# Optimization experiments

Hardware: AMD Instinct MI355X
Metric: run time of the kernel (lower is better)

Reference implementation:

```python
import jax, jax.numpy as jnp
import numpy as np

D_MODEL = 256
N_LAYERS = 2
EXPAND = 2
D_INNER = EXPAND * D_MODEL  # 512
D_STATE = 16
D_CONV = 4
DT_RANK = max(1, D_MODEL // 16)  # 16


def _selective_scan(x, dt, B, C, A, D):
    # x, dt: [b, l, d]   B, C: [b, l, n]   A: [d, n]   D: [d]
    dA = jnp.exp(jnp.einsum('bld,dn->bldn', dt, A))          # discretized state matrix
    dBx = jnp.einsum('bld,bln,bld->bldn', dt, B, x)           # dt * B * u

    def step(h, inp):
        dA_t, dBx_t, C_t = inp                                 # [b,d,n],[b,d,n],[b,n]
        h = dA_t * h + dBx_t
        y = jnp.einsum('bdn,bn->bd', h, C_t)
        return h, y

    h0 = jnp.zeros((x.shape[0], A.shape[0], A.shape[1]), x.dtype)
    _, ys = jax.lax.scan(step, h0, (jnp.moveaxis(dA, 1, 0),
                                    jnp.moveaxis(dBx, 1, 0),
                                    jnp.moveaxis(C, 1, 0)))
    return jnp.moveaxis(ys, 0, 1) + x * D                      # [b, l, d]


def _mamba_block(z, in_w, conv_w, conv_b, xp_w, dt_w, dt_b, A_log, Dp, out_w):
    b, l, _ = z.shape
    xz = z @ in_w.T                                            # [b, l, 2*d_inner]
    x, gate = jnp.split(xz, 2, axis=-1)
    # causal depthwise conv1d over time
    xt = jnp.transpose(x, (0, 2, 1))                            # [b, d_inner, l]
    xt = jax.lax.conv_general_dilated(
        xt, conv_w[:, None, :], window_strides=(1,),
        padding=[(D_CONV - 1, 0)], feature_group_count=D_INNER)
    x = jax.nn.silu(jnp.transpose(xt, (0, 2, 1)) + conv_b)      # [b, l, d_inner]
    x_dbl = x @ xp_w.T                                          # [b, l, dt_rank + 2*d_state]
    dt, Bm, Cm = jnp.split(x_dbl, [DT_RANK, DT_RANK + D_STATE], axis=-1)
    dt = jax.nn.softplus(dt @ dt_w.T + dt_b)                    # [b, l, d_inner]
    A = -jnp.exp(A_log)                                         # [d_inner, d_state]
    y = _selective_scan(x, dt, Bm, Cm, A, Dp)
    y = y * jax.nn.silu(gate)
    return y @ out_w.T                                          # [b, l, d_model]


def setup_inputs() -> dict:
    key = jax.random.key(0)
    ks = jax.random.split(key, 9)
    B, L = 2, 4096
    z = jax.random.normal(ks[0], (B, L, D_MODEL), jnp.float32)
    s = 0.02
    in_proj_w = jax.random.normal(ks[1], (N_LAYERS, 2 * D_INNER, D_MODEL), jnp.float32) * s
    conv_w = jax.random.normal(ks[2], (N_LAYERS, D_INNER, D_CONV), jnp.float32) * 0.2
    conv_b = jnp.zeros((N_LAYERS, D_INNER), jnp.float32)
    x_proj_w = jax.random.normal(ks[3], (N_LAYERS, DT_RANK + 2 * D_STATE, D_INNER), jnp.float32) * s
    dt_proj_w = jax.random.normal(ks[4], (N_LAYERS, D_INNER, DT_RANK), jnp.float32) * 0.1
    dt_proj_b = jax.random.uniform(ks[5], (N_LAYERS, D_INNER), jnp.float32, -4.0, -2.0)
    A_log = jnp.log(jnp.broadcast_to(jnp.arange(1, D_STATE + 1, dtype=jnp.float32),
                                     (N_LAYERS, D_INNER, D_STATE)))
    D_param = jnp.ones((N_LAYERS, D_INNER), jnp.float32)
    out_proj_w = jax.random.normal(ks[6], (N_LAYERS, D_MODEL, D_INNER), jnp.float32) * s
    return {"z": z, "in_proj_w": in_proj_w, "conv_w": conv_w, "conv_b": conv_b,
            "x_proj_w": x_proj_w, "dt_proj_w": dt_proj_w, "dt_proj_b": dt_proj_b,
            "A_log": A_log, "D_param": D_param, "out_proj_w": out_proj_w}


def reference(z, in_proj_w, conv_w, conv_b, x_proj_w, dt_proj_w, dt_proj_b,
              A_log, D_param, out_proj_w):
    for i in range(N_LAYERS):
        z = _mamba_block(z, in_proj_w[i], conv_w[i], conv_b[i], x_proj_w[i],
                         dt_proj_w[i], dt_proj_b[i], A_log[i], D_param[i], out_proj_w[i])
    return z
```

## Files before the change

### kernel.cpp

```cpp
#include <hip/hip_runtime.h>
#include <hip/hip_bf16.h>
#include <cstdint>
#include <cstddef>

#define DM   256
#define DI   512
#define DS   16
#define LSEQ 4096
#define BATCH 2
#define BLROWS (BATCH * LSEQ)
#define NCH  256
#define CLEN 16
#define NSC  16
#define XCP  520
#define ASP  264

typedef __bf16 bf16x8 __attribute__((ext_vector_type(8)));
typedef float  f32x4  __attribute__((ext_vector_type(4)));
typedef unsigned short u16;
typedef u16 u16x8 __attribute__((ext_vector_type(8)));

__device__ __forceinline__ u16 f2bfu(float f) {
    union { float f; unsigned u; } c; c.f = f;
    unsigned u = c.u;
    return (u16)((u + 0x7fffu + ((u >> 16) & 1u)) >> 16);
}
__device__ __forceinline__ float bfu2f(u16 u) {
    union { unsigned u; float f; } c; c.u = ((unsigned)u) << 16; return c.f;
}
__device__ __forceinline__ float siluf(float v) {
    return v * (1.0f / (1.0f + __expf(-v)));
}

#define N_INW  (2*1024*256)
#define N_OUTW (2*256*512)
#define N_XPW  (2*64*512)
#define N_Z    (BLROWS*DM)
__global__ __launch_bounds__(256) void cast_all_k(
    const float* __restrict__ in_w, const float* __restrict__ out_w,
    const float* __restrict__ xp_w, const float* __restrict__ z,
    u16* __restrict__ inw_bf, u16* __restrict__ outw_bf,
    u16* __restrict__ xpw_bf, u16* __restrict__ z_bf) {
    int i = blockIdx.x * 256 + threadIdx.x;
    if (i < N_INW) {
        inw_bf[i] = f2bfu(in_w[i]);
    } else if (i < N_INW + N_OUTW) {
        int j = i - N_INW;
        outw_bf[j] = f2bfu(out_w[j]);
    } else if (i < N_INW + N_OUTW + N_XPW) {
        int j = i - (N_INW + N_OUTW);
        int k = j & 511, o = (j >> 9) & 63, l = j >> 15;
        xpw_bf[j] = f2bfu((o < 48) ? xp_w[(l * 48 + o) * 512 + k] : 0.0f);
    } else {
        int j = i - (N_INW + N_OUTW + N_XPW);
        z_bf[j] = f2bfu(z[j]);
    }
}

__global__ __launch_bounds__(256, 2) void gemm_in_k(
    const __bf16* __restrict__ A, const __bf16* __restrict__ B,
    u16* __restrict__ Cb) {
    __shared__ u16 As[64 * ASP];
    int tid = threadIdx.x, wave = tid >> 6, lane = tid & 63;
    int bm = blockIdx.x * 64, bn = blockIdx.y * 256 + wave * 64;
    int row = lane & 15, q = lane >> 4;

    {
        int col = (tid & 31) * 8;
        #pragma unroll
        for (int i = 0; i < 8; ++i) {
            int r = i * 8 + (tid >> 5);
            u16x8 v = *(const u16x8*)((const u16*)A + (size_t)(bm + r) * 256 + col);
            *(u16x8*)&As[r * ASP + col] = v;
        }
    }
    __syncthreads();

    f32x4 acc[4][4] = {};
    for (int k = 0; k < 8; ++k) {
        bf16x8 af[4], bfr[4];
        #pragma unroll
        for (int mi = 0; mi < 4; ++mi)
            af[mi] = *(const bf16x8*)&As[(mi*16 + row) * ASP + k*32 + q*8];
        #pragma unroll
        for (int ni = 0; ni < 4; ++ni)
            bfr[ni] = *(const bf16x8*)(B + (size_t)(bn + ni*16 + row) * 256 + k*32 + q*8);
        #pragma unroll
        for (int mi = 0; mi < 4; ++mi)
            #pragma unroll
            for (int ni = 0; ni < 4; ++ni)
                acc[mi][ni] = __builtin_amdgcn_mfma_f32_16x16x32_bf16(
                    af[mi], bfr[ni], acc[mi][ni], 0, 0, 0);
    }
    #pragma unroll
    for (int mi = 0; mi < 4; ++mi)
        #pragma unroll
        for (int r = 0; r < 4; ++r) {
            size_t gr = (size_t)(bm + mi*16 + q*4 + r) * 1024;
            #pragma unroll
            for (int ni = 0; ni < 4; ++ni)
                Cb[gr + bn + ni*16 + row] = f2bfu(acc[mi][ni][r]);
        }
}

__global__ __launch_bounds__(512, 4) void fused_a_k(
    const u16* __restrict__ xz, const float* __restrict__ cw,
    const float* __restrict__ cb, const __bf16* __restrict__ xpw,
    const float* __restrict__ dtw, const float* __restrict__ dtb,
    const float* __restrict__ Alog,
    u16* __restrict__ xcb, u16* __restrict__ dtob,
    float* __restrict__ BCg, u16* __restrict__ Pb, u16* __restrict__ Sb) {
    __shared__ u16 xc_s[CLEN * XCP];
    __shared__ float xd_h[2][CLEN * 68];
    int tid = threadIdx.x;
    int c = blockIdx.x, b = blockIdx.y;
    int flat = b * NCH + c;
    int bl0 = b * LSEQ + c * CLEN;
    int d = tid;

    {
        float w0 = cw[d*4], w1 = cw[d*4+1], w2 = cw[d*4+2], w3 = cw[d*4+3];
        float bias = cb[d];
        float xm3 = 0.f, xm2 = 0.f, xm1 = 0.f;
        int l0 = c * CLEN;
        if (l0 - 3 >= 0) xm3 = bfu2f(xz[(size_t)(bl0 - 3) * 1024 + d]);
        if (l0 - 2 >= 0) xm2 = bfu2f(xz[(size_t)(bl0 - 2) * 1024 + d]);
        if (l0 - 1 >= 0) xm1 = bfu2f(xz[(size_t)(bl0 - 1) * 1024 + d]);
        #pragma unroll 4
        for (int t = 0; t < CLEN; ++t) {
            float xcur = bfu2f(xz[(size_t)(bl0 + t) * 1024 + d]);
            float acc = fmaf(w0, xm3, fmaf(w1, xm2, fmaf(w2, xm1, fmaf(w3, xcur, bias))));
            float v = siluf(acc);
            u16 vb = f2bfu(v);
            xc_s[t * XCP + d] = vb;
            xcb[(size_t)(bl0 + t) * DI + d] = vb;
            xm3 = xm2; xm2 = xm1; xm1 = xcur;
        }
    }
    __syncthreads();

    {
        int wave = tid >> 6, lane = tid & 63;
        int row = lane & 15, q = lane >> 4;
        int nt = wave & 3, kh = wave >> 2;
        f32x4 acc = {0.f, 0.f, 0.f, 0.f};
        #pragma unroll
        for (int kb = 0; kb < 8; ++kb) {
            int kk = (kh*8 + kb) * 32;
            bf16x8 a = *(const bf16x8*)&xc_s[row * XCP + kk + q*8];
            bf16x8 bb = *(const bf16x8*)(xpw + (size_t)(nt*16 + row) * 512 + kk + q*8);
            acc = __builtin_amdgcn_mfma_f32_16x16x32_bf16(a, bb, acc, 0, 0, 0);
        }
        #pragma unroll
        for (int r = 0; r < 4; ++r)
            xd_h[kh][(q*4 + r) * 68 + nt*16 + row] = acc[r];
    }
    __syncthreads();
    for (int j = tid; j < CLEN * 68; j += 512) xd_h[0][j] += xd_h[1][j];
    __syncthreads();

    {
        int t = tid >> 5, cc = tid & 31;
        BCg[(size_t)flat * (CLEN*32) + tid] = xd_h[0][t*68 + 16 + cc];
    }

    {
        float dtwr[16];
        const f32x4* w4 = (const f32x4*)(dtw + (size_t)d * 16);
        #pragma unroll
        for (int g = 0; g < 4; ++g) { f32x4 v = w4[g];
            dtwr[g*4] = v[0]; dtwr[g*4+1] = v[1]; dtwr[g*4+2] = v[2]; dtwr[g*4+3] = v[3]; }
        float dtbv = dtb[d];
        float Ac[16];
        const f32x4* a4 = (const f32x4*)(Alog + (size_t)d * 16);
        #pragma unroll
        for (int g = 0; g < 4; ++g) { f32x4 v = a4[g];
            #pragma unroll
            for (int j = 0; j < 4; ++j) Ac[g*4+j] = -__expf(v[j]); }
        bool fastp = true;
        #pragma unroll
        for (int n = 1; n < 16; ++n)
            fastp = fastp && (fabsf(Ac[n] - (float)(n+1) * Ac[0])
                              <= 1e-4f * fabsf(Ac[n]));
        float p[16], s[16];
        #pragma unroll
        for (int n = 0; n < 16; ++n) { p[n] = 1.0f; s[n] = 0.0f; }
        for (int t = 0; t < CLEN; ++t) {
            float acc = dtbv;
            #pragma unroll
            for (int r = 0; r < 16; ++r) acc = fmaf(xd_h[0][t*68 + r], dtwr[r], acc);
            float dtraw = (acc > 20.0f) ? acc : logf(1.0f + __expf(acc));
            float dtv = bfu2f(f2bfu(dtraw));
            dtob[(size_t)(bl0 + t) * DI + d] = f2bfu(dtraw);
            float xv = bfu2f(xc_s[t * XCP + d]);
            float dx = dtv * xv;
            float an[16];
            if (fastp) {
                float a0 = __expf(dtv * Ac[0]);
                an[0] = a0;
                #pragma unroll
                for (int n = 1; n < 16; ++n) an[n] = an[n-1] * a0;
            } else {
                #pragma unroll
                for (int n = 0; n < 16; ++n) an[n] = __expf(dtv * Ac[n]);
            }
            #pragma unroll
            for (int n = 0; n < 16; ++n) {
                s[n] = fmaf(an[n], s[n], xd_h[0][t*68 + 16 + n] * dx);
                p[n] *= an[n];
            }
        }
        size_t base = ((size_t)flat * DI + d) * 16;
        u16x8 pv0, pv1, sv0, sv1;
        #pragma unroll
        for (int n = 0; n < 8; ++n) {
            pv0[n] = f2bfu(p[n]);   pv1[n] = f2bfu(p[8+n]);
            sv0[n] = f2bfu(s[n]);   sv1[n] = f2bfu(s[8+n]);
        }
        *(u16x8*)(Pb + base)     = pv0;  *(u16x8*)(Pb + base + 8) = pv1;
        *(u16x8*)(Sb + base)     = sv0;  *(u16x8*)(Sb + base + 8) = sv1;
    }
}

__global__ __launch_bounds__(256) void scan1_k(
    const u16* __restrict__ Pb, const u16* __restrict__ Sb,
    float* __restrict__ Pagg, float* __restrict__ Sagg) {
    int gid = blockIdx.x * 256 + threadIdx.x;
    int scg = gid >> 13, elow = gid & 8191;
    int b = scg >> 4, sc = scg & 15;
    int cbase = b * NCH + sc * 16;
    float h = 0.f, p = 1.f;
    #pragma unroll
    for (int k = 0; k < 16; ++k) {
        size_t a = (size_t)(cbase + k) * 8192 + elow;
        float Pv = bfu2f(Pb[a]), Sv = bfu2f(Sb[a]);
        h = fmaf(Pv, h, Sv);
        p *= Pv;
    }
    Pagg[(size_t)scg * 8192 + elow] = p;
    Sagg[(size_t)scg * 8192 + elow] = h;
}

__global__ __launch_bounds__(256) void scan2_k(
    const u16* __restrict__ Pb, const u16* __restrict__ Sb,
    const float* __restrict__ Pagg, const float* __restrict__ Sagg,
    u16* __restrict__ Hg) {
    int gid = blockIdx.x * 256 + threadIdx.x;
    int scg = gid >> 13, elow = gid & 8191;
    int b = scg >> 4, sc = scg & 15;
    int cbase = b * NCH + sc * 16;
    float h = 0.f;
    for (int s2 = 0; s2 < sc; ++s2) {
        size_t ai = (size_t)(b*16 + s2) * 8192 + elow;
        h = fmaf(Pagg[ai], h, Sagg[ai]);
    }
    #pragma unroll
    for (int k = 0; k < 16; ++k) {
        size_t a = (size_t)(cbase + k) * 8192 + elow;
        Hg[a] = f2bfu(h);
        h = fmaf(bfu2f(Pb[a]), h, bfu2f(Sb[a]));
    }
}

__global__ __launch_bounds__(512, 4) void fused_c_k(
    const u16* __restrict__ xcb, const u16* __restrict__ dtob,
    const float* __restrict__ BCg, const u16* __restrict__ Hg,
    const float* __restrict__ Alog, const float* __restrict__ Dp,
    const u16* __restrict__ xz, const __bf16* __restrict__ outw,
    u16* __restrict__ Ob, float* __restrict__ Of) {
    __shared__ u16 y_s[CLEN * XCP];
    __shared__ float BCs[CLEN * 32];
    int tid = threadIdx.x;
    int c = blockIdx.x, b = blockIdx.y;
    int flat = b * NCH + c;
    int bl0 = b * LSEQ + c * CLEN;
    int d = tid;

    BCs[tid] = BCg[(size_t)flat * (CLEN*32) + tid];

    float Ac[16], h[16];
    {
        const f32x4* a4 = (const f32x4*)(Alog + (size_t)d * 16);
        const u16* h8 = Hg + ((size_t)flat * DI + d) * 16;
        u16x8 hv0 = *(const u16x8*)h8;
        u16x8 hv1 = *(const u16x8*)(h8 + 8);
        #pragma unroll
        for (int g = 0; g < 4; ++g) {
            f32x4 av = a4[g];
            #pragma unroll
            for (int j = 0; j < 4; ++j) Ac[g*4+j] = -__expf(av[j]);
        }
        #pragma unroll
        for (int n = 0; n < 8; ++n) { h[n] = bfu2f(hv0[n]); h[8+n] = bfu2f(hv1[n]); }
    }
    bool fastp = true;
    #pragma unroll
    for (int n = 1; n < 16; ++n)
        fastp = fastp && (fabsf(Ac[n] - (float)(n+1) * Ac[0]) <= 1e-4f * fabsf(Ac[n]));
    float Dv = Dp[d];
    __syncthreads();

    #pragma unroll 4
    for (int t = 0; t < CLEN; ++t) {
        float dtv = bfu2f(dtob[(size_t)(bl0 + t) * DI + d]);
        float xv  = bfu2f(xcb[(size_t)(bl0 + t) * DI + d]);
        float gv  = bfu2f(xz[(size_t)(bl0 + t) * 1024 + DI + d]);
        float dx = dtv * xv;
        float an[16];
        if (fastp) {
            float a0 = __expf(dtv * Ac[0]);
            an[0] = a0;
            #pragma unroll
            for (int n = 1; n < 16; ++n) an[n] = an[n-1] * a0;
        } else {
            #pragma unroll
            for (int n = 0; n < 16; ++n) an[n] = __expf(dtv * Ac[n]);
        }
        float y = 0.f;
        #pragma unroll
        for (int n = 0; n < 16; ++n) {
            h[n] = fmaf(an[n], h[n], BCs[t*32 + n] * dx);
            y = fmaf(h[n], BCs[t*32 + 16 + n], y);
        }
        float yv = fmaf(xv, Dv, y) * siluf(gv);
        y_s[t * XCP + d] = f2bfu(yv);
    }
    __syncthreads();

    {
        int wave = tid >> 6, lane = tid & 63;
        int row = lane & 15, q = lane >> 4;
        f32x4 acc[2] = {};
        #pragma unroll
        for (int kb = 0; kb < 16; ++kb) {
            bf16x8 a = *(const bf16x8*)&y_s[row * XCP + kb*32 + q*8];
            #pragma unroll
            for (int ni = 0; ni < 2; ++ni) {
                bf16x8 bb = *(const bf16x8*)(outw +
                    (size_t)(wave*32 + ni*16 + row) * 512 + kb*32 + q*8);
                acc[ni] = __builtin_amdgcn_mfma_f32_16x16x32_bf16(a, bb, acc[ni], 0, 0, 0);
            }
        }
        #pragma unroll
        for (int r = 0; r < 4; ++r) {
            size_t gr = (size_t)(bl0 + q*4 + r) * DM;
            #pragma unroll
            for (int ni = 0; ni < 2; ++ni) {
                int gc = wave*32 + ni*16 + row;
                if (Ob) Ob[gr + gc] = f2bfu(acc[ni][r]);
                else    Of[gr + gc] = acc[ni][r];
            }
        }
    }
}

extern "C" void kernel_launch(void* const* d_in, const int* in_sizes, int n_in,
                              void* d_out, int out_size, void* d_ws, size_t ws_size,
                              hipStream_t stream) {
    (void)in_sizes; (void)n_in; (void)out_size; (void)ws_size;
    const float* z_in   = (const float*)d_in[0];
    const float* in_w   = (const float*)d_in[1];
    const float* conv_w = (const float*)d_in[2];
    const float* conv_b = (const float*)d_in[3];
    const float* xp_w   = (const float*)d_in[4];
    const float* dt_w   = (const float*)d_in[5];
    const float* dt_b   = (const float*)d_in[6];
    const float* A_log  = (const float*)d_in[7];
    const float* D_par  = (const float*)d_in[8];
    const float* out_w  = (const float*)d_in[9];
    float* outp = (float*)d_out;

    char* p = (char*)d_ws;
    auto alloc = [&](size_t bytes) { char* r = p; p += (bytes + 255) & ~(size_t)255; return r; };
    u16* z_bf    = (u16*)alloc((size_t)BLROWS*DM*2);
    u16* z2_bf   = (u16*)alloc((size_t)BLROWS*DM*2);
    u16* xz_bf   = (u16*)alloc((size_t)BLROWS*1024*2);
    u16* xc_bf   = (u16*)alloc((size_t)BLROWS*DI*2);
    u16* dt_bf   = (u16*)alloc((size_t)BLROWS*DI*2);
    u16* inw_bf  = (u16*)alloc((size_t)2*1024*256*2);
    u16* outw_bf = (u16*)alloc((size_t)2*256*512*2);
    u16* xpw_bf  = (u16*)alloc((size_t)2*64*512*2);
    float* BCg   = (float*)alloc((size_t)BATCH*NCH*CLEN*32*4);
    u16* Pbuf    = (u16*)alloc((size_t)BATCH*NCH*DI*DS*2);
    u16* Sbuf    = (u16*)alloc((size_t)BATCH*NCH*DI*DS*2);
    u16* Hbuf    = (u16*)alloc((size_t)BATCH*NCH*DI*DS*2);
    float* PaggG = (float*)alloc((size_t)BATCH*NSC*8192*4);
    float* SaggG = (float*)alloc((size_t)BATCH*NSC*8192*4);

    cast_all_k<<<(N_INW + N_OUTW + N_XPW + N_Z)/256, 256, 0, stream>>>(
        in_w, out_w, xp_w, z_in, inw_bf, outw_bf, xpw_bf, z_bf);

    const u16* zcur = z_bf;
    for (int l = 0; l < 2; ++l) {
        gemm_in_k<<<dim3(BLROWS/64, 1024/256), 256, 0, stream>>>(
            (const __bf16*)zcur, (const __bf16*)(inw_bf + (size_t)l*1024*256),
            xz_bf);
        fused_a_k<<<dim3(NCH, BATCH), 512, 0, stream>>>(
            xz_bf, conv_w + (size_t)l*DI*4, conv_b + (size_t)l*DI,
            (const __bf16*)(xpw_bf + (size_t)l*64*512),
            dt_w + (size_t)l*DI*16, dt_b + (size_t)l*DI,
            A_log + (size_t)l*DI*DS,
            xc_bf, dt_bf, BCg, Pbuf, Sbuf);
        scan1_k<<<BATCH*NSC*8192/256, 256, 0, stream>>>(Pbuf, Sbuf, PaggG, SaggG);
        scan2_k<<<BATCH*NSC*8192/256, 256, 0, stream>>>(Pbuf, Sbuf, PaggG, SaggG, Hbuf);
        fused_c_k<<<dim3(NCH, BATCH), 512, 0, stream>>>(
            xc_bf, dt_bf, BCg, Hbuf,
            A_log + (size_t)l*DI*DS, D_par + (size_t)l*DI,
            xz_bf, (const __bf16*)(outw_bf + (size_t)l*256*512),
            (l == 0) ? z2_bf : nullptr, (l == 1) ? outp : nullptr);
        zcur = z2_bf;
    }
}
```

Before: 234.5 us.

## Split fused scan kernels into separate conv, GEMM, dt, scan stages

Breaks the two large fused per-chunk kernels into separate conv, x-projection GEMM, dt, chunk-scan and output-GEMM kernels. It also halves the chunk length and doubles the chunk count, splits channels across two blocks per chunk, and computes the chunk decay product in closed form from the summed dt with a power tree. The aim is more parallel blocks, lower register pressure and shorter serial dependency chains. In exchange it adds extra launches and global round-trips for xd and the y intermediate, and doubles the chunk-state buffers that scan1/scan2 must process.

```diff
diff --git a/kernel.cpp b/kernel.cpp
--- a/kernel.cpp
+++ b/kernel.cpp
@@ -9,10 +9,9 @@
 #define LSEQ 4096
 #define BATCH 2
 #define BLROWS (BATCH * LSEQ)
-#define NCH  256
-#define CLEN 16
-#define NSC  16
-#define XCP  520
+#define NCH  512
+#define CLEN 8
+#define NSC  32
 #define ASP  264
 
 typedef __bf16 bf16x8 __attribute__((ext_vector_type(8)));
@@ -31,6 +30,13 @@
 __device__ __forceinline__ float siluf(float v) {
     return v * (1.0f / (1.0f + __expf(-v)));
 }
+
+#define POW_TREE(an, e1)                                                     \
+    {   float e2 = (e1)*(e1), e4 = e2*e2, e8 = e4*e4;                        \
+        an[0]=(e1); an[1]=e2; an[2]=e2*(e1); an[3]=e4; an[4]=e4*(e1);        \
+        an[5]=e4*e2; an[6]=e4*an[2]; an[7]=e8; an[8]=e8*(e1); an[9]=e8*e2;   \
+        an[10]=e8*an[2]; an[11]=e8*e4; an[12]=e8*an[4]; an[13]=e8*an[5];     \
+        an[14]=e8*an[6]; an[15]=e8*e8; }
 
 #define N_INW  (2*1024*256)
 #define N_OUTW (2*256*512)
@@ -64,7 +70,6 @@
     int tid = threadIdx.x, wave = tid >> 6, lane = tid & 63;
     int bm = blockIdx.x * 64, bn = blockIdx.y * 256 + wave * 64;
     int row = lane & 15, q = lane >> 4;
-
     {
         int col = (tid & 31) * 8;
         #pragma unroll
@@ -75,7 +80,6 @@
         }
     }
     __syncthreads();
-
     f32x4 acc[4][4] = {};
     for (int k = 0; k < 8; ++k) {
         bf16x8 af[4], bfr[4];
@@ -103,123 +107,137 @@
         }
 }
 
-__global__ __launch_bounds__(512, 4) void fused_a_k(
+__global__ __launch_bounds__(256) void conv_k(
     const u16* __restrict__ xz, const float* __restrict__ cw,
-    const float* __restrict__ cb, const __bf16* __restrict__ xpw,
-    const float* __restrict__ dtw, const float* __restrict__ dtb,
-    const float* __restrict__ Alog,
-    u16* __restrict__ xcb, u16* __restrict__ dtob,
-    float* __restrict__ BCg, u16* __restrict__ Pb, u16* __restrict__ Sb) {
-    __shared__ u16 xc_s[CLEN * XCP];
-    __shared__ float xd_h[2][CLEN * 68];
+    const float* __restrict__ cb, u16* __restrict__ xc) {
+    int gid = blockIdx.x * 256 + threadIdx.x;
+    int d = gid & 511;
+    int row0 = (gid >> 9) * 8;
+    int l0 = row0 & 4095;
+    float w0 = cw[d*4], w1 = cw[d*4+1], w2 = cw[d*4+2], w3 = cw[d*4+3];
+    float bias = cb[d];
+    float xm3 = (l0 >= 3) ? bfu2f(xz[(size_t)(row0-3)*1024 + d]) : 0.f;
+    float xm2 = (l0 >= 2) ? bfu2f(xz[(size_t)(row0-2)*1024 + d]) : 0.f;
+    float xm1 = (l0 >= 1) ? bfu2f(xz[(size_t)(row0-1)*1024 + d]) : 0.f;
+    #pragma unroll
+    for (int t = 0; t < 8; ++t) {
+        float xcur = bfu2f(xz[(size_t)(row0+t)*1024 + d]);
+        float a = fmaf(w0, xm3, fmaf(w1, xm2, fmaf(w2, xm1, fmaf(w3, xcur, bias))));
+        xc[(size_t)(row0+t)*512 + d] = f2bfu(siluf(a));
+        xm3 = xm2; xm2 = xm1; xm1 = xcur;
+    }
+}
+
+__global__ __launch_bounds__(256) void gemm_xd_k(
+    const __bf16* __restrict__ xc, const __bf16* __restrict__ xpw,
+    float* __restrict__ xd) {
+    int tid = threadIdx.x, wave = tid >> 6, lane = tid & 63;
+    int bm = blockIdx.x * 16;
+    int row = lane & 15, q = lane >> 4;
+    f32x4 acc = {};
+    #pragma unroll
+    for (int k = 0; k < 16; ++k) {
+        bf16x8 a = *(const bf16x8*)(xc + (size_t)(bm + row)*512 + k*32 + q*8);
+        bf16x8 b = *(const bf16x8*)(xpw + (size_t)(wave*16 + row)*512 + k*32 + q*8);
+        acc = __builtin_amdgcn_mfma_f32_16x16x32_bf16(a, b, acc, 0, 0, 0);
+    }
+    #pragma unroll
+    for (int r = 0; r < 4; ++r)
+        xd[(size_t)(bm + q*4 + r)*64 + wave*16 + row] = acc[r];
+}
+
+__global__ __launch_bounds__(256) void dt_k(
+    const float* __restrict__ xd, const float* __restrict__ dtw,
+    const float* __restrict__ dtb, u16* __restrict__ dt) {
+    int gid = blockIdx.x * 256 + threadIdx.x;
+    int d = gid & 511, t = gid >> 9;
+    const f32x4* w4 = (const f32x4*)(dtw + (size_t)d*16);
+    const f32x4* x4 = (const f32x4*)(xd + (size_t)t*64);
+    float acc = dtb[d];
+    #pragma unroll
+    for (int g = 0; g < 4; ++g) {
+        f32x4 wv = w4[g], xv = x4[g];
+        #pragma unroll
+        for (int j = 0; j < 4; ++j) acc = fmaf(xv[j], wv[j], acc);
+    }
+    float dtraw = (acc > 20.0f) ? acc : __logf(1.0f + __expf(acc));
+    dt[gid] = f2bfu(dtraw);
+}
+
+__global__ __launch_bounds__(256, 6) void scan_ps_k(
+    const u16* __restrict__ xc, const u16* __restrict__ dt,
+    const float* __restrict__ xd, const float* __restrict__ Alog,
+    u16* __restrict__ Pb, u16* __restrict__ Sb) {
+    __shared__ float BCs[CLEN * 32];
     int tid = threadIdx.x;
-    int c = blockIdx.x, b = blockIdx.y;
+    int c = blockIdx.x, bh = blockIdx.y;
+    int b = bh >> 1, dch = (bh & 1) * 256 + tid;
     int flat = b * NCH + c;
     int bl0 = b * LSEQ + c * CLEN;
-    int d = tid;
-
+    BCs[tid] = xd[(size_t)(bl0 + (tid >> 5)) * 64 + 16 + (tid & 31)];
+    float Ac0; bool fastp = true;
     {
-        float w0 = cw[d*4], w1 = cw[d*4+1], w2 = cw[d*4+2], w3 = cw[d*4+3];
-        float bias = cb[d];
-        float xm3 = 0.f, xm2 = 0.f, xm1 = 0.f;
-        int l0 = c * CLEN;
-        if (l0 - 3 >= 0) xm3 = bfu2f(xz[(size_t)(bl0 - 3) * 1024 + d]);
-        if (l0 - 2 >= 0) xm2 = bfu2f(xz[(size_t)(bl0 - 2) * 1024 + d]);
-        if (l0 - 1 >= 0) xm1 = bfu2f(xz[(size_t)(bl0 - 1) * 1024 + d]);
-        #pragma unroll 4
+        const f32x4* a4 = (const f32x4*)(Alog + (size_t)dch * 16);
+        f32x4 v0 = a4[0];
+        Ac0 = -__expf(v0[0]);
+        #pragma unroll
+        for (int g = 0; g < 4; ++g) { f32x4 v = a4[g];
+            #pragma unroll
+            for (int j = 0; j < 4; ++j) { int n = g*4 + j; if (n) {
+                float acn = -__expf(v[j]);
+                fastp = fastp && (fabsf(acn - (float)(n+1)*Ac0) <= 1e-4f*fabsf(acn));
+            } } }
+    }
+    __syncthreads();
+    float s[16];
+    #pragma unroll
+    for (int n = 0; n < 16; ++n) s[n] = 0.f;
+    float Sdt = 0.f;
+    if (fastp) {
+        #pragma unroll
         for (int t = 0; t < CLEN; ++t) {
-            float xcur = bfu2f(xz[(size_t)(bl0 + t) * 1024 + d]);
-            float acc = fmaf(w0, xm3, fmaf(w1, xm2, fmaf(w2, xm1, fmaf(w3, xcur, bias))));
-            float v = siluf(acc);
-            u16 vb = f2bfu(v);
-            xc_s[t * XCP + d] = vb;
-            xcb[(size_t)(bl0 + t) * DI + d] = vb;
-            xm3 = xm2; xm2 = xm1; xm1 = xcur;
-        }
-    }
-    __syncthreads();
-
-    {
-        int wave = tid >> 6, lane = tid & 63;
-        int row = lane & 15, q = lane >> 4;
-        int nt = wave & 3, kh = wave >> 2;
-        f32x4 acc = {0.f, 0.f, 0.f, 0.f};
-        #pragma unroll
-        for (int kb = 0; kb < 8; ++kb) {
-            int kk = (kh*8 + kb) * 32;
-            bf16x8 a = *(const bf16x8*)&xc_s[row * XCP + kk + q*8];
-            bf16x8 bb = *(const bf16x8*)(xpw + (size_t)(nt*16 + row) * 512 + kk + q*8);
-            acc = __builtin_amdgcn_mfma_f32_16x16x32_bf16(a, bb, acc, 0, 0, 0);
-        }
-        #pragma unroll
-        for (int r = 0; r < 4; ++r)
-            xd_h[kh][(q*4 + r) * 68 + nt*16 + row] = acc[r];
-    }
-    __syncthreads();
-    for (int j = tid; j < CLEN * 68; j += 512) xd_h[0][j] += xd_h[1][j];
-    __syncthreads();
-
-    {
-        int t = tid >> 5, cc = tid & 31;
-        BCg[(size_t)flat * (CLEN*32) + tid] = xd_h[0][t*68 + 16 + cc];
-    }
-
-    {
-        float dtwr[16];
-        const f32x4* w4 = (const f32x4*)(dtw + (size_t)d * 16);
-        #pragma unroll
-        for (int g = 0; g < 4; ++g) { f32x4 v = w4[g];
-            dtwr[g*4] = v[0]; dtwr[g*4+1] = v[1]; dtwr[g*4+2] = v[2]; dtwr[g*4+3] = v[3]; }
-        float dtbv = dtb[d];
-        float Ac[16];
-        const f32x4* a4 = (const f32x4*)(Alog + (size_t)d * 16);
-        #pragma unroll
-        for (int g = 0; g < 4; ++g) { f32x4 v = a4[g];
-            #pragma unroll
-            for (int j = 0; j < 4; ++j) Ac[g*4+j] = -__expf(v[j]); }
-        bool fastp = true;
-        #pragma unroll
-        for (int n = 1; n < 16; ++n)
-            fastp = fastp && (fabsf(Ac[n] - (float)(n+1) * Ac[0])
-                              <= 1e-4f * fabsf(Ac[n]));
-        float p[16], s[16];
-        #pragma unroll
-        for (int n = 0; n < 16; ++n) { p[n] = 1.0f; s[n] = 0.0f; }
+            float dtv = bfu2f(dt[(size_t)(bl0+t)*512 + dch]);
+            float xv  = bfu2f(xc[(size_t)(bl0+t)*512 + dch]);
+            float dx = dtv * xv;
+            Sdt += dtv;
+            float e1 = __expf(dtv * Ac0);
+            float an[16];
+            POW_TREE(an, e1)
+            #pragma unroll
+            for (int n = 0; n < 16; ++n)
+                s[n] = fmaf(an[n], s[n], BCs[t*32 + n] * dx);
+        }
+    } else {
         for (int t = 0; t < CLEN; ++t) {
-            float acc = dtbv;
-            #pragma unroll
-            for (int r = 0; r < 16; ++r) acc = fmaf(xd_h[0][t*68 + r], dtwr[r], acc);
-            float dtraw = (acc > 20.0f) ? acc : logf(1.0f + __expf(acc));
-            float dtv = bfu2f(f2bfu(dtraw));
-            dtob[(size_t)(bl0 + t) * DI + d] = f2bfu(dtraw);
-            float xv = bfu2f(xc_s[t * XCP + d]);
+            float dtv = bfu2f(dt[(size_t)(bl0+t)*512 + dch]);
+            float xv  = bfu2f(xc[(size_t)(bl0+t)*512 + dch]);
             float dx = dtv * xv;
-            float an[16];
-            if (fastp) {
-                float a0 = __expf(dtv * Ac[0]);
-                an[0] = a0;
-                #pragma unroll
-                for (int n = 1; n < 16; ++n) an[n] = an[n-1] * a0;
-            } else {
-                #pragma unroll
-                for (int n = 0; n < 16; ++n) an[n] = __expf(dtv * Ac[n]);
+            Sdt += dtv;
+            #pragma unroll
+            for (int n = 0; n < 16; ++n) {
+                float an = __expf(dtv * -__expf(Alog[(size_t)dch*16 + n]));
+                s[n] = fmaf(an, s[n], BCs[t*32 + n] * dx);
             }
-            #pragma unroll
-            for (int n = 0; n < 16; ++n) {
-                s[n] = fmaf(an[n], s[n], xd_h[0][t*68 + 16 + n] * dx);
-                p[n] *= an[n];
-            }
-        }
-        size_t base = ((size_t)flat * DI + d) * 16;
-        u16x8 pv0, pv1, sv0, sv1;
-        #pragma unroll
-        for (int n = 0; n < 8; ++n) {
-            pv0[n] = f2bfu(p[n]);   pv1[n] = f2bfu(p[8+n]);
-            sv0[n] = f2bfu(s[n]);   sv1[n] = f2bfu(s[8+n]);
-        }
-        *(u16x8*)(Pb + base)     = pv0;  *(u16x8*)(Pb + base + 8) = pv1;
-        *(u16x8*)(Sb + base)     = sv0;  *(u16x8*)(Sb + base + 8) = sv1;
-    }
+        }
+    }
+    float pw[16];
+    if (fastp) {
+        float E1 = __expf(Ac0 * Sdt);
+        POW_TREE(pw, E1)
+    } else {
+        #pragma unroll
+        for (int n = 0; n < 16; ++n)
+            pw[n] = __expf(-__expf(Alog[(size_t)dch*16 + n]) * Sdt);
+    }
+    size_t base = ((size_t)flat * DI + dch) * 16;
+    u16x8 pv0, pv1, sv0, sv1;
+    #pragma unroll
+    for (int n = 0; n < 8; ++n) {
+        pv0[n] = f2bfu(pw[n]);  pv1[n] = f2bfu(pw[8+n]);
+        sv0[n] = f2bfu(s[n]);   sv1[n] = f2bfu(s[8+n]);
+    }
+    *(u16x8*)(Pb + base)     = pv0;  *(u16x8*)(Pb + base + 8) = pv1;
+    *(u16x8*)(Sb + base)     = sv0;  *(u16x8*)(Sb + base + 8) = sv1;
 }
 
 __global__ __launch_bounds__(256) void scan1_k(
@@ -227,7 +245,7 @@
     float* __restrict__ Pagg, float* __restrict__ Sagg) {
     int gid = blockIdx.x * 256 + threadIdx.x;
     int scg = gid >> 13, elow = gid & 8191;
-    int b = scg >> 4, sc = scg & 15;
+    int b = scg >> 5, sc = scg & 31;
     int cbase = b * NCH + sc * 16;
     float h = 0.f, p = 1.f;
     #pragma unroll
@@ -247,11 +265,11 @@
     u16* __restrict__ Hg) {
     int gid = blockIdx.x * 256 + threadIdx.x;
     int scg = gid >> 13, elow = gid & 8191;
-    int b = scg >> 4, sc = scg & 15;
+    int b = scg >> 5, sc = scg & 31;
     int cbase = b * NCH + sc * 16;
     float h = 0.f;
     for (int s2 = 0; s2 < sc; ++s2) {
-        size_t ai = (size_t)(b*16 + s2) * 8192 + elow;
+        size_t ai = (size_t)(b*32 + s2) * 8192 + elow;
         h = fmaf(Pagg[ai], h, Sagg[ai]);
     }
     #pragma unroll
@@ -262,94 +280,110 @@
     }
 }
 
-__global__ __launch_bounds__(512, 4) void fused_c_k(
-    const u16* __restrict__ xcb, const u16* __restrict__ dtob,
-    const float* __restrict__ BCg, const u16* __restrict__ Hg,
+__global__ __launch_bounds__(256, 6) void scan_y_k(
+    const u16* __restrict__ xc, const u16* __restrict__ dt,
+    const float* __restrict__ xd, const u16* __restrict__ Hg,
     const float* __restrict__ Alog, const float* __restrict__ Dp,
-    const u16* __restrict__ xz, const __bf16* __restrict__ outw,
-    u16* __restrict__ Ob, float* __restrict__ Of) {
-    __shared__ u16 y_s[CLEN * XCP];
+    const u16* __restrict__ xz, u16* __restrict__ yg) {
     __shared__ float BCs[CLEN * 32];
     int tid = threadIdx.x;
-    int c = blockIdx.x, b = blockIdx.y;
+    int c = blockIdx.x, bh = blockIdx.y;
+    int b = bh >> 1, dch = (bh & 1) * 256 + tid;
     int flat = b * NCH + c;
     int bl0 = b * LSEQ + c * CLEN;
-    int d = tid;
-
-    BCs[tid] = BCg[(size_t)flat * (CLEN*32) + tid];
-
-    float Ac[16], h[16];
+    BCs[tid] = xd[(size_t)(bl0 + (tid >> 5)) * 64 + 16 + (tid & 31)];
+    float Ac0; bool fastp = true;
     {
-        const f32x4* a4 = (const f32x4*)(Alog + (size_t)d * 16);
-        const u16* h8 = Hg + ((size_t)flat * DI + d) * 16;
+        const f32x4* a4 = (const f32x4*)(Alog + (size_t)dch * 16);
+        f32x4 v0 = a4[0];
+        Ac0 = -__expf(v0[0]);
+        #pragma unroll
+        for (int g = 0; g < 4; ++g) { f32x4 v = a4[g];
+            #pragma unroll
+            for (int j = 0; j < 4; ++j) { int n = g*4 + j; if (n) {
+                float acn = -__expf(v[j]);
+                fastp = fastp && (fabsf(acn - (float)(n+1)*Ac0) <= 1e-4f*fabsf(acn));
+            } } }
+    }
+    float h[16];
+    {
+        const u16* h8 = Hg + ((size_t)flat * DI + dch) * 16;
         u16x8 hv0 = *(const u16x8*)h8;
         u16x8 hv1 = *(const u16x8*)(h8 + 8);
         #pragma unroll
-        for (int g = 0; g < 4; ++g) {
-            f32x4 av = a4[g];
-            #pragma unroll
-            for (int j = 0; j < 4; ++j) Ac[g*4+j] = -__expf(av[j]);
-        }
-        #pragma unroll
         for (int n = 0; n < 8; ++n) { h[n] = bfu2f(hv0[n]); h[8+n] = bfu2f(hv1[n]); }
     }
-    bool fastp = true;
-    #pragma unroll
-    for (int n = 1; n < 16; ++n)
-        fastp = fastp && (fabsf(Ac[n] - (float)(n+1) * Ac[0]) <= 1e-4f * fabsf(Ac[n]));
-    float Dv = Dp[d];
+    float Dv = Dp[dch];
     __syncthreads();
-
-    #pragma unroll 4
-    for (int t = 0; t < CLEN; ++t) {
-        float dtv = bfu2f(dtob[(size_t)(bl0 + t) * DI + d]);
-        float xv  = bfu2f(xcb[(size_t)(bl0 + t) * DI + d]);
-        float gv  = bfu2f(xz[(size_t)(bl0 + t) * 1024 + DI + d]);
-        float dx = dtv * xv;
-        float an[16];
-        if (fastp) {
-            float a0 = __expf(dtv * Ac[0]);
-            an[0] = a0;
-            #pragma unroll
-            for (int n = 1; n < 16; ++n) an[n] = an[n-1] * a0;
-        } else {
-            #pragma unroll
-            for (int n = 0; n < 16; ++n) an[n] = __expf(dtv * Ac[n]);
-        }
-        float y = 0.f;
-        #pragma unroll
-        for (int n = 0; n < 16; ++n) {
-            h[n] = fmaf(an[n], h[n], BCs[t*32 + n] * dx);
-            y = fmaf(h[n], BCs[t*32 + 16 + n], y);
-        }
-        float yv = fmaf(xv, Dv, y) * siluf(gv);
-        y_s[t * XCP + d] = f2bfu(yv);
-    }
-    __syncthreads();
-
-    {
-        int wave = tid >> 6, lane = tid & 63;
-        int row = lane & 15, q = lane >> 4;
-        f32x4 acc[2] = {};
-        #pragma unroll
-        for (int kb = 0; kb < 16; ++kb) {
-            bf16x8 a = *(const bf16x8*)&y_s[row * XCP + kb*32 + q*8];
-            #pragma unroll
-            for (int ni = 0; ni < 2; ++ni) {
-                bf16x8 bb = *(const bf16x8*)(outw +
-                    (size_t)(wave*32 + ni*16 + row) * 512 + kb*32 + q*8);
-                acc[ni] = __builtin_amdgcn_mfma_f32_16x16x32_bf16(a, bb, acc[ni], 0, 0, 0);
+    if (fastp) {
+        #pragma unroll
+        for (int t = 0; t < CLEN; ++t) {
+            float dtv = bfu2f(dt[(size_t)(bl0+t)*512 + dch]);
+            float xv  = bfu2f(xc[(size_t)(bl0+t)*512 + dch]);
+            float gv  = bfu2f(xz[(size_t)(bl0+t)*1024 + DI + dch]);
+            float dx = dtv * xv;
+            float e1 = __expf(dtv * Ac0);
+            float an[16];
+            POW_TREE(an, e1)
+            float y0 = 0.f, y1 = 0.f, y2 = 0.f, y3 = 0.f;
+            #pragma unroll
+            for (int n = 0; n < 4; ++n) {
+                h[n]    = fmaf(an[n],    h[n],    BCs[t*32 + n]    * dx);
+                h[4+n]  = fmaf(an[4+n],  h[4+n],  BCs[t*32 + 4+n]  * dx);
+                h[8+n]  = fmaf(an[8+n],  h[8+n],  BCs[t*32 + 8+n]  * dx);
+                h[12+n] = fmaf(an[12+n], h[12+n], BCs[t*32 + 12+n] * dx);
+                y0 = fmaf(h[n],    BCs[t*32 + 16 + n],    y0);
+                y1 = fmaf(h[4+n],  BCs[t*32 + 16 + 4+n],  y1);
+                y2 = fmaf(h[8+n],  BCs[t*32 + 16 + 8+n],  y2);
+                y3 = fmaf(h[12+n], BCs[t*32 + 16 + 12+n], y3);
             }
-        }
-        #pragma unroll
-        for (int r = 0; r < 4; ++r) {
-            size_t gr = (size_t)(bl0 + q*4 + r) * DM;
-            #pragma unroll
-            for (int ni = 0; ni < 2; ++ni) {
-                int gc = wave*32 + ni*16 + row;
-                if (Ob) Ob[gr + gc] = f2bfu(acc[ni][r]);
-                else    Of[gr + gc] = acc[ni][r];
+            float y = (y0 + y1) + (y2 + y3);
+            float yv = fmaf(xv, Dv, y) * siluf(gv);
+            yg[(size_t)(bl0+t)*512 + dch] = f2bfu(yv);
+        }
+    } else {
+        for (int t = 0; t < CLEN; ++t) {
+            float dtv = bfu2f(dt[(size_t)(bl0+t)*512 + dch]);
+            float xv  = bfu2f(xc[(size_t)(bl0+t)*512 + dch]);
+            float gv  = bfu2f(xz[(size_t)(bl0+t)*1024 + DI + dch]);
+            float dx = dtv * xv;
+            float y = 0.f;
+            #pragma unroll
+            for (int n = 0; n < 16; ++n) {
+                float an = __expf(dtv * -__expf(Alog[(size_t)dch*16 + n]));
+                h[n] = fmaf(an, h[n], BCs[t*32 + n] * dx);
+                y = fmaf(h[n], BCs[t*32 + 16 + n], y);
             }
+            float yv = fmaf(xv, Dv, y) * siluf(gv);
+            yg[(size_t)(bl0+t)*512 + dch] = f2bfu(yv);
+        }
+    }
+}
+
+__global__ __launch_bounds__(256) void gemm_out_k(
+    const __bf16* __restrict__ yg, const __bf16* __restrict__ outw,
+    u16* __restrict__ Ob, float* __restrict__ Of) {
+    int tid = threadIdx.x, wave = tid >> 6, lane = tid & 63;
+    int bm = blockIdx.x * 16;
+    int row = lane & 15, q = lane >> 4;
+    f32x4 acc[4] = {};
+    #pragma unroll
+    for (int k = 0; k < 16; ++k) {
+        bf16x8 a = *(const bf16x8*)(yg + (size_t)(bm + row)*512 + k*32 + q*8);
+        #pragma unroll
+        for (int ni = 0; ni < 4; ++ni) {
+            bf16x8 b = *(const bf16x8*)(outw + (size_t)(wave*64 + ni*16 + row)*512 + k*32 + q*8);
+            acc[ni] = __builtin_amdgcn_mfma_f32_16x16x32_bf16(a, b, acc[ni], 0, 0, 0);
+        }
+    }
+    #pragma unroll
+    for (int r = 0; r < 4; ++r) {
+        size_t gr = (size_t)(bm + q*4 + r) * DM;
+        #pragma unroll
+        for (int ni = 0; ni < 4; ++ni) {
+            int gc = wave*64 + ni*16 + row;
+            if (Ob) Ob[gr + gc] = f2bfu(acc[ni][r]);
+            else    Of[gr + gc] = acc[ni][r];
         }
     }
 }
@@ -377,10 +411,11 @@
     u16* xz_bf   = (u16*)alloc((size_t)BLROWS*1024*2);
     u16* xc_bf   = (u16*)alloc((size_t)BLROWS*DI*2);
     u16* dt_bf   = (u16*)alloc((size_t)BLROWS*DI*2);
+    u16* yg_bf   = (u16*)alloc((size_t)BLROWS*DI*2);
+    float* xdG   = (float*)alloc((size_t)BLROWS*64*4);
     u16* inw_bf  = (u16*)alloc((size_t)2*1024*256*2);
     u16* outw_bf = (u16*)alloc((size_t)2*256*512*2);
     u16* xpw_bf  = (u16*)alloc((size_t)2*64*512*2);
-    float* BCg   = (float*)alloc((size_t)BATCH*NCH*CLEN*32*4);
     u16* Pbuf    = (u16*)alloc((size_t)BATCH*NCH*DI*DS*2);
     u16* Sbuf    = (u16*)alloc((size_t)BATCH*NCH*DI*DS*2);
     u16* Hbuf    = (u16*)alloc((size_t)BATCH*NCH*DI*DS*2);
@@ -395,18 +430,21 @@
         gemm_in_k<<<dim3(BLROWS/64, 1024/256), 256, 0, stream>>>(
             (const __bf16*)zcur, (const __bf16*)(inw_bf + (size_t)l*1024*256),
             xz_bf);
-        fused_a_k<<<dim3(NCH, BATCH), 512, 0, stream>>>(
-            xz_bf, conv_w + (size_t)l*DI*4, conv_b + (size_t)l*DI,
-            (const __bf16*)(xpw_bf + (size_t)l*64*512),
-            dt_w + (size_t)l*DI*16, dt_b + (size_t)l*DI,
-            A_log + (size_t)l*DI*DS,
-            xc_bf, dt_bf, BCg, Pbuf, Sbuf);
+        conv_k<<<(BLROWS/8)*512/256, 256, 0, stream>>>(
+            xz_bf, conv_w + (size_t)l*DI*4, conv_b + (size_t)l*DI, xc_bf);
+        gemm_xd_k<<<BLROWS/16, 256, 0, stream>>>(
+            (const __bf16*)xc_bf, (const __bf16*)(xpw_bf + (size_t)l*64*512), xdG);
+        dt_k<<<(size_t)BLROWS*512/256, 256, 0, stream>>>(
+            xdG, dt_w + (size_t)l*DI*16, dt_b + (size_t)l*DI, dt_bf);
+        scan_ps_k<<<dim3(NCH, 2*BATCH), 256, 0, stream>>>(
+            xc_bf, dt_bf, xdG, A_log + (size_t)l*DI*DS, Pbuf, Sbuf);
         scan1_k<<<BATCH*NSC*8192/256, 256, 0, stream>>>(Pbuf, Sbuf, PaggG, SaggG);
         scan2_k<<<BATCH*NSC*8192/256, 256, 0, stream>>>(Pbuf, Sbuf, PaggG, SaggG, Hbuf);
-        fused_c_k<<<dim3(NCH, BATCH), 512, 0, stream>>>(
-            xc_bf, dt_bf, BCg, Hbuf,
-            A_log + (size_t)l*DI*DS, D_par + (size_t)l*DI,
-            xz_bf, (const __bf16*)(outw_bf + (size_t)l*256*512),
+        scan_y_k<<<dim3(NCH, 2*BATCH), 256, 0, stream>>>(
+            xc_bf, dt_bf, xdG, Hbuf,
+            A_log + (size_t)l*DI*DS, D_par + (size_t)l*DI, xz_bf, yg_bf);
+        gemm_out_k<<<BLROWS/16, 256, 0, stream>>>(
+            (const __bf16*)yg_bf, (const __bf16*)(outw_bf + (size_t)l*256*512),
             (l == 0) ? z2_bf : nullptr, (l == 1) ? outp : nullptr);
         zcur = z2_bf;
     }
```

New measurement: 335.1 us. 1.43x slower.
